# Optimization experiments

Measured on AMD Instinct MI355X. Metric: run time of the kernel, lower is better.

Reference implementation:

```python
import jax, jax.numpy as jnp
import numpy as np

B, C, CI, HM, HC = 4, 64, 32, 128, 64  # batch, in_channels, inter_channels, main HW, cross HW
BN_EPS = 1e-5


def conv1x1(x, w, b):
    # x: [B,Cin,H,W], w: [Cout,Cin], b: [Cout]
    return jnp.einsum('bchw,oc->bohw', x, w) + b[None, :, None, None]


def _lin_coords(n_in, n_out):
    # PyTorch bilinear, align_corners=False: src = (i+0.5)*scale - 0.5, clamped
    scale = n_in / n_out
    src = (jnp.arange(n_out, dtype=jnp.float32) + 0.5) * scale - 0.5
    src = jnp.clip(src, 0.0, n_in - 1)
    i0 = jnp.floor(src).astype(jnp.int32)
    i1 = jnp.minimum(i0 + 1, n_in - 1)
    w = src - i0.astype(jnp.float32)
    return i0, i1, w


def resize_bilinear(x, h_out, w_out):
    # x: [B,C,H,W] -> [B,C,h_out,w_out], matches torch F.interpolate(mode='bilinear', align_corners=False)
    _, _, h_in, w_in = x.shape
    i0, i1, wh = _lin_coords(h_in, h_out)
    x = x[:, :, i0, :] * (1.0 - wh)[None, None, :, None] + x[:, :, i1, :] * wh[None, None, :, None]
    j0, j1, ww = _lin_coords(w_in, w_out)
    x = x[:, :, :, j0] * (1.0 - ww)[None, None, None, :] + x[:, :, :, j1] * ww[None, None, None, :]
    return x


def setup_inputs() -> dict:
    key = jax.random.key(0)
    ks = jax.random.split(key, 12)
    p = lambda k, shape, s=0.05: jax.random.normal(k, shape, dtype=jnp.float32) * s
    return {
        'main_feature': jax.random.normal(ks[0], (B, C, HM, HM), dtype=jnp.float32),
        'cross_feature': jax.random.normal(ks[1], (B, C, HC, HC), dtype=jnp.float32),
        'g_w': p(ks[2], (CI, C)), 'g_b': p(ks[3], (CI,)),
        'theta_w': p(ks[4], (CI, C)), 'theta_b': p(ks[5], (CI,)),
        'phi_w': p(ks[6], (CI, C)), 'phi_b': p(ks[7], (CI,)),
        'w_w': p(ks[8], (C, CI)), 'w_b': p(ks[9], (C,)),
        'bn_gamma': 1.0 + p(ks[10], (C,)), 'bn_beta': p(ks[11], (C,)),
    }


def reference(main_feature, cross_feature, g_w, g_b, theta_w, theta_b,
              phi_w, phi_b, w_w, w_b, bn_gamma, bn_beta):
    b, _, hc, wc = cross_feature.shape
    hm = main_feature.shape[2]
    # g(cross) -> [B, Nc, Ci]
    x = conv1x1(cross_feature, g_w, g_b).reshape(b, CI, -1).transpose(0, 2, 1)
    # theta(cross) -> [B, Ci, Nc]
    y = conv1x1(cross_feature, theta_w, theta_b).reshape(b, CI, -1)
    # phi(resize(main -> cross size)) -> [B, Nc, Ci]
    z = resize_bilinear(main_feature, hc, hc)
    z = conv1x1(z, phi_w, phi_b).reshape(b, CI, -1).transpose(0, 2, 1)
    # unscaled attention: [B, Nc, Nc]
    f = jnp.einsum('bnc,bcm->bnm', x, y)
    attn = jax.nn.softmax(f, axis=-1)
    out = jnp.einsum('bnm,bmc->bnc', attn, z)           # [B, Nc, Ci]
    out = out.transpose(0, 2, 1).reshape(b, CI, hc, wc)  # [B, Ci, Hc, Wc]
    # W: 1x1 conv + BatchNorm2d (training mode: batch statistics, biased var)
    out = conv1x1(out, w_w, w_b)
    mean = out.mean(axis=(0, 2, 3), keepdims=True)
    var = out.var(axis=(0, 2, 3), keepdims=True)
    out = (out - mean) * jax.lax.rsqrt(var + BN_EPS)
    out = out * bn_gamma[None, :, None, None] + bn_beta[None, :, None, None]
    out = resize_bilinear(out, hm, hm)
    return out + main_feature
```

## Files before the change

### kernel.cpp

```cpp
#include <hip/hip_runtime.h>
#include <hip/hip_bf16.h>


typedef __attribute__((ext_vector_type(8))) short bf16x8;
typedef __attribute__((ext_vector_type(4))) float f32x4;
typedef __attribute__((ext_vector_type(16))) float f32x16;

#define LOG2E 1.4426950408889634f

static __device__ __forceinline__ unsigned short f2bf_bits(float x) {
    __hip_bfloat16 h = __float2bfloat16(x);
    return *(unsigned short*)&h;
}
static __device__ __forceinline__ unsigned int pk2bf(float a, float b) {
    __hip_bfloat162 h = __float22bfloat162_rn(make_float2(a, b));
    return *(unsigned int*)&h;
}

__global__ __launch_bounds__(256) void qkv_kernel(
    const float* __restrict__ cross, const float* __restrict__ mainf,
    const float* __restrict__ g_w,  const float* __restrict__ g_b,
    const float* __restrict__ th_w, const float* __restrict__ th_b,
    const float* __restrict__ ph_w, const float* __restrict__ ph_b,
    __hip_bfloat16* __restrict__ Qb, __hip_bfloat16* __restrict__ Kb,
    __hip_bfloat16* __restrict__ Vt)
{
    __shared__ float xs[64][128];
    const int kind = blockIdx.x >> 7;
    const int sub  = blockIdx.x & 127;
    const int b    = sub >> 5;
    const int n0   = (sub & 31) << 7;
    const int tid  = threadIdx.x;
    const float* w  = (kind == 0) ? g_w : (kind == 1) ? th_w : ph_w;
    const float* bs = (kind == 0) ? g_b : (kind == 1) ? th_b : ph_b;

    if (kind < 2) {
        const float* src = cross + (((size_t)(b * 64)) << 12) + n0;
        const int jr = (tid & 31) << 2, c0 = tid >> 5;
#pragma unroll
        for (int it = 0; it < 8; ++it) {
            int c = (it << 3) | c0;
            *(float4*)&xs[c][jr] = *(const float4*)(src + ((size_t)c << 12) + jr);
        }
    } else {
        const int px = tid & 127, chh = tid >> 7;
        const int n = n0 + px;
        const int i2 = (n >> 6) << 1, j2 = (n & 63) << 1;
        const float* src = mainf + (((size_t)(b * 64)) << 14) + i2 * 128 + j2;
#pragma unroll 4
        for (int cc = 0; cc < 32; ++cc) {
            int c = (chh << 5) | cc;
            const float2 a = *(const float2*)(src + ((size_t)c << 14));
            const float2 d = *(const float2*)(src + ((size_t)c << 14) + 128);
            xs[c][px] = 0.25f * ((a.x + a.y) + (d.x + d.y));
        }
    }
    __syncthreads();

    const int px = tid & 127, cih = tid >> 7, ci0 = cih << 4;
    float acc[16];
#pragma unroll
    for (int j = 0; j < 16; ++j) acc[j] = bs[ci0 + j];
#pragma unroll 4
    for (int c = 0; c < 64; ++c) {
        float x = xs[c][px];
#pragma unroll
        for (int j = 0; j < 16; ++j)
            acc[j] = fmaf(w[((ci0 + j) << 6) + c], x, acc[j]);
    }
    const int n = n0 + px;
    const int pix = (b << 12) + n;
    if (kind < 2) {
        if (kind == 0) {
#pragma unroll
            for (int j = 0; j < 16; ++j) acc[j] *= LOG2E;
        }
        unsigned int u[8];
#pragma unroll
        for (int i = 0; i < 8; ++i)
            u[i] = (unsigned int)f2bf_bits(acc[2 * i]) |
                   ((unsigned int)f2bf_bits(acc[2 * i + 1]) << 16);
        uint4* d4 = (uint4*)(((kind == 0) ? Qb : Kb) + (size_t)pix * 32 + ci0);
        d4[0] = make_uint4(u[0], u[1], u[2], u[3]);
        d4[1] = make_uint4(u[4], u[5], u[6], u[7]);
    } else {
#pragma unroll
        for (int j = 0; j < 16; ++j)
            Vt[((size_t)((b << 5) | (ci0 + j)) << 12) + n] = __float2bfloat16(acc[j]);
    }
}

__global__ __launch_bounds__(256) void attn_part(
    const __hip_bfloat16* __restrict__ Qb, const __hip_bfloat16* __restrict__ Kb,
    const __hip_bfloat16* __restrict__ Vt,
    float* __restrict__ pnum, float* __restrict__ pden)
{
    __shared__ __align__(16) float redbuf[3][64][20];
    const int tid = threadIdx.x, lane = tid & 63, w = tid >> 6;
    const int q = lane & 31, h = lane >> 5;
    const int b = blockIdx.y, qbase = blockIdx.x << 5, half = blockIdx.z;
    const int sig = (q & ~12) | ((q & 4) << 1) | ((q & 8) >> 1);

    const __hip_bfloat16* Qrow = Qb + (((size_t)(b << 12) + qbase + q) << 5);
    const bf16x8 bq1 = *(const bf16x8*)(Qrow + 8 * h);
    const bf16x8 bq2 = *(const bf16x8*)(Qrow + 16 + 8 * h);

    const __hip_bfloat16* Kbb = Kb + ((size_t)(b << 12) << 5);
    const __hip_bfloat16* Vbb = Vt + ((size_t)(b << 5) << 12) + ((size_t)q << 12);
    const int kq = (half << 11) + (w << 9);
#define LDK1(k) (*(const bf16x8*)(Kbb + ((size_t)((k) + sig) << 5) + 8 * h))
#define LDK2(k) (*(const bf16x8*)(Kbb + ((size_t)((k) + sig) << 5) + 16 + 8 * h))
#define LDV1(k) (*(const bf16x8*)(Vbb + (k) + 8 * h))
#define LDV2(k) (*(const bf16x8*)(Vbb + (k) + 16 + 8 * h))

    f32x16 acc;
#pragma unroll
    for (int r = 0; r < 16; ++r) acc[r] = 0.f;
    const f32x16 z16 = acc;
    float den = 0.f;

    bf16x8 a1c = LDK1(kq),      a2c = LDK2(kq);
    bf16x8 v1B = LDV1(kq),      v2B = LDV2(kq);
    bf16x8 a1n = LDK1(kq + 32), a2n = LDK2(kq + 32);
    bf16x8 v1N = LDV1(kq + 32), v2N = LDV2(kq + 32);
    bf16x8 ap1, ap2, v1A, v2A;

    {
        f32x16 s = __builtin_amdgcn_mfma_f32_32x32x16_bf16(a1c, bq1, z16, 0, 0, 0);
        s = __builtin_amdgcn_mfma_f32_32x32x16_bf16(a2c, bq2, s, 0, 0, 0);
        float e[16];
#pragma unroll
        for (int r = 0; r < 16; ++r) e[r] = __builtin_amdgcn_exp2f(s[r]);
        den += (((e[0]+e[1])+(e[2]+e[3])) + ((e[4]+e[5])+(e[6]+e[7])))
             + (((e[8]+e[9])+(e[10]+e[11])) + ((e[12]+e[13])+(e[14]+e[15])));
        uint4 t1 = make_uint4(pk2bf(e[0],e[1]), pk2bf(e[2],e[3]),
                              pk2bf(e[4],e[5]), pk2bf(e[6],e[7]));
        uint4 t2 = make_uint4(pk2bf(e[8],e[9]), pk2bf(e[10],e[11]),
                              pk2bf(e[12],e[13]), pk2bf(e[14],e[15]));
        ap1 = *(bf16x8*)&t1; ap2 = *(bf16x8*)&t2;
    }

#pragma unroll 2
    for (int ch = 1; ch < 16; ++ch) {
        const int kn = kq + ((ch + 1) & 15) * 32;
        v1A = v1B; v2A = v2B;
        v1B = v1N; v2B = v2N;
        a1c = a1n; a2c = a2n;
        a1n = LDK1(kn); a2n = LDK2(kn);
        v1N = LDV1(kn); v2N = LDV2(kn);

        f32x16 s = __builtin_amdgcn_mfma_f32_32x32x16_bf16(a1c, bq1, z16, 0, 0, 0);
        s = __builtin_amdgcn_mfma_f32_32x32x16_bf16(a2c, bq2, s, 0, 0, 0);

        acc = __builtin_amdgcn_mfma_f32_32x32x16_bf16(ap1, v1A, acc, 0, 0, 0);
        acc = __builtin_amdgcn_mfma_f32_32x32x16_bf16(ap2, v2A, acc, 0, 0, 0);

        float e[16];
#pragma unroll
        for (int r = 0; r < 16; ++r) e[r] = __builtin_amdgcn_exp2f(s[r]);
        den += (((e[0]+e[1])+(e[2]+e[3])) + ((e[4]+e[5])+(e[6]+e[7])))
             + (((e[8]+e[9])+(e[10]+e[11])) + ((e[12]+e[13])+(e[14]+e[15])));
        uint4 t1 = make_uint4(pk2bf(e[0],e[1]), pk2bf(e[2],e[3]),
                              pk2bf(e[4],e[5]), pk2bf(e[6],e[7]));
        uint4 t2 = make_uint4(pk2bf(e[8],e[9]), pk2bf(e[10],e[11]),
                              pk2bf(e[12],e[13]), pk2bf(e[14],e[15]));
        ap1 = *(bf16x8*)&t1; ap2 = *(bf16x8*)&t2;
    }
    acc = __builtin_amdgcn_mfma_f32_32x32x16_bf16(ap1, v1B, acc, 0, 0, 0);
    acc = __builtin_amdgcn_mfma_f32_32x32x16_bf16(ap2, v2B, acc, 0, 0, 0);
#undef LDK1
#undef LDK2
#undef LDV1
#undef LDV2

    den += __shfl_xor(den, 32);

    if (w) {
        float* rb = &redbuf[w - 1][lane][0];
        f32x4* rb4 = (f32x4*)rb;
#pragma unroll
        for (int p = 0; p < 4; ++p) {
            f32x4 t = {acc[4*p], acc[4*p+1], acc[4*p+2], acc[4*p+3]};
            rb4[p] = t;
        }
        rb[16] = den;
    }
    __syncthreads();
    if (w == 0) {
#pragma unroll
        for (int ww = 0; ww < 3; ++ww) {
            const float* rb = &redbuf[ww][lane][0];
            const f32x4* rb4 = (const f32x4*)rb;
#pragma unroll
            for (int p = 0; p < 4; ++p) {
                f32x4 t = rb4[p];
                acc[4*p] += t[0]; acc[4*p+1] += t[1];
                acc[4*p+2] += t[2]; acc[4*p+3] += t[3];
            }
            den += rb[16];
        }
        const int tile = (((half << 2) | b) << 7) | blockIdx.x;
        float* pn = pnum + ((size_t)tile << 10);
#pragma unroll
        for (int r = 0; r < 16; ++r) {
            int qr = (r & 3) + 8 * (r >> 2) + 4 * h;
            pn[(qr << 5) + q] = acc[r];
        }
        if (h == 0) pden[(tile << 5) + q] = den;
    }
}

__global__ __launch_bounds__(256) void attn_combine(
    const float* __restrict__ pnum, const float* __restrict__ pden,
    const float* __restrict__ w_w, const float* __restrict__ w_b,
    float* __restrict__ out2)
{
    __shared__ __align__(16) float obuf[32][36];
    const int tid = threadIdx.x;
    const int b = blockIdx.y, qbase = blockIdx.x << 5;
    const int tile0 = ((b) << 7) | blockIdx.x;
    const int tile1 = ((4 + b) << 7) | blockIdx.x;

    const float* pn0 = pnum + ((size_t)tile0 << 10);
    const float* pn1 = pnum + ((size_t)tile1 << 10);
#pragma unroll
    for (int k = 0; k < 4; ++k) {
        int e = tid + (k << 8);
        int qr = e >> 5, ci = e & 31;
        float num = pn0[e] + pn1[e];
        float den = pden[(tile0 << 5) + qr] + pden[(tile1 << 5) + qr];
        obuf[qr][ci] = num * (1.0f / den);
    }
    __syncthreads();

    const int qq = tid & 31, cog = tid >> 5;
    float ov[32];
    const float4* orow = (const float4*)&obuf[qq][0];
#pragma unroll
    for (int k4 = 0; k4 < 8; ++k4) {
        float4 t = orow[k4];
        ov[4*k4] = t.x; ov[4*k4+1] = t.y; ov[4*k4+2] = t.z; ov[4*k4+3] = t.w;
    }
    float* dstbase = out2 + (((size_t)(b << 6)) << 12) + qbase + qq;
#pragma unroll
    for (int kk = 0; kk < 8; ++kk) {
        int co = (kk << 3) | cog;
        const float4* wr = (const float4*)&w_w[co << 5];
        float acc2 = w_b[co];
#pragma unroll
        for (int k4 = 0; k4 < 8; ++k4) {
            float4 t = wr[k4];
            acc2 = fmaf(t.x, ov[4*k4],   acc2);
            acc2 = fmaf(t.y, ov[4*k4+1], acc2);
            acc2 = fmaf(t.z, ov[4*k4+2], acc2);
            acc2 = fmaf(t.w, ov[4*k4+3], acc2);
        }
        dstbase[(size_t)co << 12] = acc2;
    }
}

__global__ __launch_bounds__(256) void stats_kernel(
    const float* __restrict__ out2, float* __restrict__ stats1)
{
    int co = blockIdx.x >> 2, b = blockIdx.x & 3, t = threadIdx.x;
    const float* p = out2 + ((size_t)((b << 6) | co) << 12);
    float s = 0.f, s2 = 0.f;
#pragma unroll
    for (int ii = 0; ii < 16; ++ii) {
        float v = p[(ii << 8) | t];
        s += v; s2 = fmaf(v, v, s2);
    }
    __shared__ float rs[256], rs2[256];
    rs[t] = s; rs2[t] = s2;
    __syncthreads();
    for (int off = 128; off > 0; off >>= 1) {
        if (t < off) { rs[t] += rs[t + off]; rs2[t] += rs2[t + off]; }
        __syncthreads();
    }
    if (t == 0) {
        stats1[blockIdx.x * 2]     = rs[0];
        stats1[blockIdx.x * 2 + 1] = rs2[0];
    }
}

__global__ __launch_bounds__(256) void up_kernel(
    const float* __restrict__ out2, const float* __restrict__ stats1,
    const float* __restrict__ gamma, const float* __restrict__ beta,
    const float* __restrict__ mainf, float* __restrict__ out)
{
    int gid = blockIdx.x * 256 + threadIdx.x;
    int j4 = (gid & 31) << 2;
    int i  = (gid >> 5) & 127;
    int co = (gid >> 12) & 63;
    int b  = gid >> 18;

    float sm = 0.f, sq = 0.f;
#pragma unroll
    for (int bb = 0; bb < 4; ++bb) {
        sm += stats1[((co << 2) | bb) * 2];
        sq += stats1[((co << 2) | bb) * 2 + 1];
    }
    float mean = sm * (1.0f / 16384.0f);
    float var  = sq * (1.0f / 16384.0f) - mean * mean;
    float inv  = rsqrtf(var + 1e-5f);
    float scale = gamma[co] * inv;
    float shift = beta[co] - mean * scale;

    int ih = i >> 1;
    int k0, k1; float wi;
    if (i & 1)       { k0 = ih;     k1 = (ih < 63) ? ih + 1 : 63; wi = 0.25f; }
    else if (ih == 0){ k0 = 0;      k1 = 0;                       wi = 0.0f;  }
    else             { k0 = ih - 1; k1 = ih;                      wi = 0.75f; }

    const float* p0r = out2 + ((size_t)((b << 6) | co) << 12) + (k0 << 6);
    const float* p1r = out2 + ((size_t)((b << 6) | co) << 12) + (k1 << 6);

    float res[4];
#pragma unroll
    for (int jj = 0; jj < 4; ++jj) {
        int j = j4 | jj;
        int il = j >> 1;
        int l0, l1; float wj;
        if (j & 1)       { l0 = il;     l1 = (il < 63) ? il + 1 : 63; wj = 0.25f; }
        else if (il == 0){ l0 = 0;      l1 = 0;                       wj = 0.0f;  }
        else             { l0 = il - 1; l1 = il;                      wj = 0.75f; }
        float v00 = p0r[l0], v01 = p0r[l1];
        float v10 = p1r[l0], v11 = p1r[l1];
        float top = v00 + wj * (v01 - v00);
        float bot = v10 + wj * (v11 - v10);
        float v = top + wi * (bot - top);
        res[jj] = fmaf(v, scale, shift);
    }
    size_t idx = (((size_t)((b << 6) | co)) << 14) + (i << 7) + j4;
    float4 m4 = *(const float4*)(mainf + idx);
    *(float4*)(out + idx) = make_float4(res[0] + m4.x, res[1] + m4.y,
                                        res[2] + m4.z, res[3] + m4.w);
}

extern "C" void kernel_launch(void* const* d_in, const int* in_sizes, int n_in,
                              void* d_out, int out_size, void* d_ws, size_t ws_size,
                              hipStream_t stream)
{
    const float* mainf = (const float*)d_in[0];
    const float* cross = (const float*)d_in[1];
    const float* g_w   = (const float*)d_in[2];
    const float* g_b   = (const float*)d_in[3];
    const float* th_w  = (const float*)d_in[4];
    const float* th_b  = (const float*)d_in[5];
    const float* ph_w  = (const float*)d_in[6];
    const float* ph_b  = (const float*)d_in[7];
    const float* w_w   = (const float*)d_in[8];
    const float* w_b   = (const float*)d_in[9];
    const float* gamma = (const float*)d_in[10];
    const float* beta  = (const float*)d_in[11];
    float* out = (float*)d_out;

    __hip_bfloat16* Qb = (__hip_bfloat16*)d_ws;
    __hip_bfloat16* Kb = Qb + 524288;
    __hip_bfloat16* Vt = Kb + 524288;
    float* out2   = (float*)(Vt + 524288);
    float* stats1 = out2 + 1048576;
    float* pnum   = stats1 + 512;
    float* pden   = pnum + 1048576;

    qkv_kernel<<<384, 256, 0, stream>>>(cross, mainf, g_w, g_b, th_w, th_b,
                                        ph_w, ph_b, Qb, Kb, Vt);
    attn_part<<<dim3(128, 4, 2), 256, 0, stream>>>(Qb, Kb, Vt, pnum, pden);
    attn_combine<<<dim3(128, 4), 256, 0, stream>>>(pnum, pden, w_w, w_b, out2);
    stats_kernel<<<256, 256, 0, stream>>>(out2, stats1);
    up_kernel<<<4096, 256, 0, stream>>>(out2, stats1, gamma, beta, mainf, out);
}
```

Baseline: 151.8 us.

## Process two query tiles per attention block and fold BN stats into combine via atomics

The attention partial kernel now handles 64 queries per block in two 32-row tiles that share each K/V load, which halves K/V traffic and the grid size. The separate BN statistics kernel is removed: attn_combine reduces per-channel sum and sum-of-squares with wave shuffles and atomically adds them into a buffer that qkv_kernel zeroes. This saves a kernel launch and a reread of out2, at the cost of higher register pressure in attn_part, fewer blocks in flight, and nondeterministic float atomic ordering.

```diff
diff --git a/kernel.cpp b/kernel.cpp
--- a/kernel.cpp
+++ b/kernel.cpp
@@ -15,6 +15,21 @@
 static __device__ __forceinline__ unsigned int pk2bf(float a, float b) {
     __hip_bfloat162 h = __float22bfloat162_rn(make_float2(a, b));
     return *(unsigned int*)&h;
+}
+
+static __device__ __forceinline__ void softmax_pack(
+    const f32x16& s, float& den, bf16x8& ap1, bf16x8& ap2)
+{
+    float e[16];
+#pragma unroll
+    for (int r = 0; r < 16; ++r) e[r] = __builtin_amdgcn_exp2f(s[r]);
+    den += (((e[0]+e[1])+(e[2]+e[3])) + ((e[4]+e[5])+(e[6]+e[7])))
+         + (((e[8]+e[9])+(e[10]+e[11])) + ((e[12]+e[13])+(e[14]+e[15])));
+    uint4 t1 = make_uint4(pk2bf(e[0],e[1]), pk2bf(e[2],e[3]),
+                          pk2bf(e[4],e[5]), pk2bf(e[6],e[7]));
+    uint4 t2 = make_uint4(pk2bf(e[8],e[9]), pk2bf(e[10],e[11]),
+                          pk2bf(e[12],e[13]), pk2bf(e[14],e[15]));
+    ap1 = *(bf16x8*)&t1; ap2 = *(bf16x8*)&t2;
 }
 
 __global__ __launch_bounds__(256) void qkv_kernel(
@@ -23,7 +38,7 @@
     const float* __restrict__ th_w, const float* __restrict__ th_b,
     const float* __restrict__ ph_w, const float* __restrict__ ph_b,
     __hip_bfloat16* __restrict__ Qb, __hip_bfloat16* __restrict__ Kb,
-    __hip_bfloat16* __restrict__ Vt)
+    __hip_bfloat16* __restrict__ Vt, float* __restrict__ stats1)
 {
     __shared__ float xs[64][128];
     const int kind = blockIdx.x >> 7;
@@ -33,6 +48,8 @@
     const int tid  = threadIdx.x;
     const float* w  = (kind == 0) ? g_w : (kind == 1) ? th_w : ph_w;
     const float* bs = (kind == 0) ? g_b : (kind == 1) ? th_b : ph_b;
+
+    if (blockIdx.x == 0 && tid < 128) stats1[tid] = 0.f;
 
     if (kind < 2) {
         const float* src = cross + (((size_t)(b * 64)) << 12) + n0;
@@ -98,12 +115,15 @@
     __shared__ __align__(16) float redbuf[3][64][20];
     const int tid = threadIdx.x, lane = tid & 63, w = tid >> 6;
     const int q = lane & 31, h = lane >> 5;
-    const int b = blockIdx.y, qbase = blockIdx.x << 5, half = blockIdx.z;
+    const int b = blockIdx.y, qbase = blockIdx.x << 6, half = blockIdx.z;
     const int sig = (q & ~12) | ((q & 4) << 1) | ((q & 8) >> 1);
 
-    const __hip_bfloat16* Qrow = Qb + (((size_t)(b << 12) + qbase + q) << 5);
-    const bf16x8 bq1 = *(const bf16x8*)(Qrow + 8 * h);
-    const bf16x8 bq2 = *(const bf16x8*)(Qrow + 16 + 8 * h);
+    const __hip_bfloat16* QrowA = Qb + (((size_t)(b << 12) + qbase + q) << 5);
+    const bf16x8 bq1A = *(const bf16x8*)(QrowA + 8 * h);
+    const bf16x8 bq2A = *(const bf16x8*)(QrowA + 16 + 8 * h);
+    const __hip_bfloat16* QrowB = QrowA + (32 << 5);
+    const bf16x8 bq1B = *(const bf16x8*)(QrowB + 8 * h);
+    const bf16x8 bq2B = *(const bf16x8*)(QrowB + 16 + 8 * h);
 
     const __hip_bfloat16* Kbb = Kb + ((size_t)(b << 12) << 5);
     const __hip_bfloat16* Vbb = Vt + ((size_t)(b << 5) << 12) + ((size_t)q << 12);
@@ -113,77 +133,72 @@
 #define LDV1(k) (*(const bf16x8*)(Vbb + (k) + 8 * h))
 #define LDV2(k) (*(const bf16x8*)(Vbb + (k) + 16 + 8 * h))
 
-    f32x16 acc;
-#pragma unroll
-    for (int r = 0; r < 16; ++r) acc[r] = 0.f;
-    const f32x16 z16 = acc;
-    float den = 0.f;
+    f32x16 accA, accB;
+#pragma unroll
+    for (int r = 0; r < 16; ++r) { accA[r] = 0.f; accB[r] = 0.f; }
+    const f32x16 z16 = accA;
+    float denA = 0.f, denB = 0.f;
 
     bf16x8 a1c = LDK1(kq),      a2c = LDK2(kq);
-    bf16x8 v1B = LDV1(kq),      v2B = LDV2(kq);
+    bf16x8 vb1 = LDV1(kq),      vb2 = LDV2(kq);
     bf16x8 a1n = LDK1(kq + 32), a2n = LDK2(kq + 32);
-    bf16x8 v1N = LDV1(kq + 32), v2N = LDV2(kq + 32);
-    bf16x8 ap1, ap2, v1A, v2A;
+    bf16x8 vn1 = LDV1(kq + 32), vn2 = LDV2(kq + 32);
+    bf16x8 apA1, apA2, apB1, apB2, vp1, vp2;
 
     {
-        f32x16 s = __builtin_amdgcn_mfma_f32_32x32x16_bf16(a1c, bq1, z16, 0, 0, 0);
-        s = __builtin_amdgcn_mfma_f32_32x32x16_bf16(a2c, bq2, s, 0, 0, 0);
-        float e[16];
-#pragma unroll
-        for (int r = 0; r < 16; ++r) e[r] = __builtin_amdgcn_exp2f(s[r]);
-        den += (((e[0]+e[1])+(e[2]+e[3])) + ((e[4]+e[5])+(e[6]+e[7])))
-             + (((e[8]+e[9])+(e[10]+e[11])) + ((e[12]+e[13])+(e[14]+e[15])));
-        uint4 t1 = make_uint4(pk2bf(e[0],e[1]), pk2bf(e[2],e[3]),
-                              pk2bf(e[4],e[5]), pk2bf(e[6],e[7]));
-        uint4 t2 = make_uint4(pk2bf(e[8],e[9]), pk2bf(e[10],e[11]),
-                              pk2bf(e[12],e[13]), pk2bf(e[14],e[15]));
-        ap1 = *(bf16x8*)&t1; ap2 = *(bf16x8*)&t2;
+        f32x16 sA = __builtin_amdgcn_mfma_f32_32x32x16_bf16(a1c, bq1A, z16, 0, 0, 0);
+        sA = __builtin_amdgcn_mfma_f32_32x32x16_bf16(a2c, bq2A, sA, 0, 0, 0);
+        f32x16 sB = __builtin_amdgcn_mfma_f32_32x32x16_bf16(a1c, bq1B, z16, 0, 0, 0);
+        sB = __builtin_amdgcn_mfma_f32_32x32x16_bf16(a2c, bq2B, sB, 0, 0, 0);
+        softmax_pack(sA, denA, apA1, apA2);
+        softmax_pack(sB, denB, apB1, apB2);
     }
 
 #pragma unroll 2
     for (int ch = 1; ch < 16; ++ch) {
         const int kn = kq + ((ch + 1) & 15) * 32;
-        v1A = v1B; v2A = v2B;
-        v1B = v1N; v2B = v2N;
+        vp1 = vb1; vp2 = vb2;
+        vb1 = vn1; vb2 = vn2;
         a1c = a1n; a2c = a2n;
         a1n = LDK1(kn); a2n = LDK2(kn);
-        v1N = LDV1(kn); v2N = LDV2(kn);
-
-        f32x16 s = __builtin_amdgcn_mfma_f32_32x32x16_bf16(a1c, bq1, z16, 0, 0, 0);
-        s = __builtin_amdgcn_mfma_f32_32x32x16_bf16(a2c, bq2, s, 0, 0, 0);
-
-        acc = __builtin_amdgcn_mfma_f32_32x32x16_bf16(ap1, v1A, acc, 0, 0, 0);
-        acc = __builtin_amdgcn_mfma_f32_32x32x16_bf16(ap2, v2A, acc, 0, 0, 0);
-
-        float e[16];
-#pragma unroll
-        for (int r = 0; r < 16; ++r) e[r] = __builtin_amdgcn_exp2f(s[r]);
-        den += (((e[0]+e[1])+(e[2]+e[3])) + ((e[4]+e[5])+(e[6]+e[7])))
-             + (((e[8]+e[9])+(e[10]+e[11])) + ((e[12]+e[13])+(e[14]+e[15])));
-        uint4 t1 = make_uint4(pk2bf(e[0],e[1]), pk2bf(e[2],e[3]),
-                              pk2bf(e[4],e[5]), pk2bf(e[6],e[7]));
-        uint4 t2 = make_uint4(pk2bf(e[8],e[9]), pk2bf(e[10],e[11]),
-                              pk2bf(e[12],e[13]), pk2bf(e[14],e[15]));
-        ap1 = *(bf16x8*)&t1; ap2 = *(bf16x8*)&t2;
-    }
-    acc = __builtin_amdgcn_mfma_f32_32x32x16_bf16(ap1, v1B, acc, 0, 0, 0);
-    acc = __builtin_amdgcn_mfma_f32_32x32x16_bf16(ap2, v2B, acc, 0, 0, 0);
+        vn1 = LDV1(kn); vn2 = LDV2(kn);
+
+        f32x16 sA = __builtin_amdgcn_mfma_f32_32x32x16_bf16(a1c, bq1A, z16, 0, 0, 0);
+        sA = __builtin_amdgcn_mfma_f32_32x32x16_bf16(a2c, bq2A, sA, 0, 0, 0);
+        f32x16 sB = __builtin_amdgcn_mfma_f32_32x32x16_bf16(a1c, bq1B, z16, 0, 0, 0);
+        sB = __builtin_amdgcn_mfma_f32_32x32x16_bf16(a2c, bq2B, sB, 0, 0, 0);
+
+        accA = __builtin_amdgcn_mfma_f32_32x32x16_bf16(apA1, vp1, accA, 0, 0, 0);
+        accA = __builtin_amdgcn_mfma_f32_32x32x16_bf16(apA2, vp2, accA, 0, 0, 0);
+        accB = __builtin_amdgcn_mfma_f32_32x32x16_bf16(apB1, vp1, accB, 0, 0, 0);
+        accB = __builtin_amdgcn_mfma_f32_32x32x16_bf16(apB2, vp2, accB, 0, 0, 0);
+
+        softmax_pack(sA, denA, apA1, apA2);
+        softmax_pack(sB, denB, apB1, apB2);
+    }
+    accA = __builtin_amdgcn_mfma_f32_32x32x16_bf16(apA1, vb1, accA, 0, 0, 0);
+    accA = __builtin_amdgcn_mfma_f32_32x32x16_bf16(apA2, vb2, accA, 0, 0, 0);
+    accB = __builtin_amdgcn_mfma_f32_32x32x16_bf16(apB1, vb1, accB, 0, 0, 0);
+    accB = __builtin_amdgcn_mfma_f32_32x32x16_bf16(apB2, vb2, accB, 0, 0, 0);
 #undef LDK1
 #undef LDK2
 #undef LDV1
 #undef LDV2
 
-    den += __shfl_xor(den, 32);
+    denA += __shfl_xor(denA, 32);
+    denB += __shfl_xor(denB, 32);
+
+    const int tileA = (((half << 2) | b) << 7) | (blockIdx.x << 1);
 
     if (w) {
         float* rb = &redbuf[w - 1][lane][0];
         f32x4* rb4 = (f32x4*)rb;
 #pragma unroll
         for (int p = 0; p < 4; ++p) {
-            f32x4 t = {acc[4*p], acc[4*p+1], acc[4*p+2], acc[4*p+3]};
+            f32x4 t = {accA[4*p], accA[4*p+1], accA[4*p+2], accA[4*p+3]};
             rb4[p] = t;
         }
-        rb[16] = den;
+        rb[16] = denA;
     }
     __syncthreads();
     if (w == 0) {
@@ -194,26 +209,59 @@
 #pragma unroll
             for (int p = 0; p < 4; ++p) {
                 f32x4 t = rb4[p];
-                acc[4*p] += t[0]; acc[4*p+1] += t[1];
-                acc[4*p+2] += t[2]; acc[4*p+3] += t[3];
+                accA[4*p] += t[0]; accA[4*p+1] += t[1];
+                accA[4*p+2] += t[2]; accA[4*p+3] += t[3];
             }
-            den += rb[16];
-        }
-        const int tile = (((half << 2) | b) << 7) | blockIdx.x;
-        float* pn = pnum + ((size_t)tile << 10);
+            denA += rb[16];
+        }
+        float* pn = pnum + ((size_t)tileA << 10);
 #pragma unroll
         for (int r = 0; r < 16; ++r) {
             int qr = (r & 3) + 8 * (r >> 2) + 4 * h;
-            pn[(qr << 5) + q] = acc[r];
-        }
-        if (h == 0) pden[(tile << 5) + q] = den;
+            pn[(qr << 5) + q] = accA[r];
+        }
+        if (h == 0) pden[(tileA << 5) + q] = denA;
+    }
+    __syncthreads();
+
+    if (w) {
+        float* rb = &redbuf[w - 1][lane][0];
+        f32x4* rb4 = (f32x4*)rb;
+#pragma unroll
+        for (int p = 0; p < 4; ++p) {
+            f32x4 t = {accB[4*p], accB[4*p+1], accB[4*p+2], accB[4*p+3]};
+            rb4[p] = t;
+        }
+        rb[16] = denB;
+    }
+    __syncthreads();
+    if (w == 0) {
+#pragma unroll
+        for (int ww = 0; ww < 3; ++ww) {
+            const float* rb = &redbuf[ww][lane][0];
+            const f32x4* rb4 = (const f32x4*)rb;
+#pragma unroll
+            for (int p = 0; p < 4; ++p) {
+                f32x4 t = rb4[p];
+                accB[4*p] += t[0]; accB[4*p+1] += t[1];
+                accB[4*p+2] += t[2]; accB[4*p+3] += t[3];
+            }
+            denB += rb[16];
+        }
+        float* pn = pnum + ((size_t)(tileA | 1) << 10);
+#pragma unroll
+        for (int r = 0; r < 16; ++r) {
+            int qr = (r & 3) + 8 * (r >> 2) + 4 * h;
+            pn[(qr << 5) + q] = accB[r];
+        }
+        if (h == 0) pden[((tileA | 1) << 5) + q] = denB;
     }
 }
 
 __global__ __launch_bounds__(256) void attn_combine(
     const float* __restrict__ pnum, const float* __restrict__ pden,
     const float* __restrict__ w_w, const float* __restrict__ w_b,
-    float* __restrict__ out2)
+    float* __restrict__ out2, float* __restrict__ stats1)
 {
     __shared__ __align__(16) float obuf[32][36];
     const int tid = threadIdx.x;
@@ -256,30 +304,16 @@
             acc2 = fmaf(t.w, ov[4*k4+3], acc2);
         }
         dstbase[(size_t)co << 12] = acc2;
-    }
-}
-
-__global__ __launch_bounds__(256) void stats_kernel(
-    const float* __restrict__ out2, float* __restrict__ stats1)
-{
-    int co = blockIdx.x >> 2, b = blockIdx.x & 3, t = threadIdx.x;
-    const float* p = out2 + ((size_t)((b << 6) | co) << 12);
-    float s = 0.f, s2 = 0.f;
-#pragma unroll
-    for (int ii = 0; ii < 16; ++ii) {
-        float v = p[(ii << 8) | t];
-        s += v; s2 = fmaf(v, v, s2);
-    }
-    __shared__ float rs[256], rs2[256];
-    rs[t] = s; rs2[t] = s2;
-    __syncthreads();
-    for (int off = 128; off > 0; off >>= 1) {
-        if (t < off) { rs[t] += rs[t + off]; rs2[t] += rs2[t + off]; }
-        __syncthreads();
-    }
-    if (t == 0) {
-        stats1[blockIdx.x * 2]     = rs[0];
-        stats1[blockIdx.x * 2 + 1] = rs2[0];
+        float s1 = acc2, s2 = acc2 * acc2;
+#pragma unroll
+        for (int m = 1; m < 32; m <<= 1) {
+            s1 += __shfl_xor(s1, m);
+            s2 += __shfl_xor(s2, m);
+        }
+        if (qq == 0) {
+            atomicAdd(&stats1[co << 1], s1);
+            atomicAdd(&stats1[(co << 1) | 1], s2);
+        }
     }
 }
 
@@ -294,12 +328,8 @@
     int co = (gid >> 12) & 63;
     int b  = gid >> 18;
 
-    float sm = 0.f, sq = 0.f;
-#pragma unroll
-    for (int bb = 0; bb < 4; ++bb) {
-        sm += stats1[((co << 2) | bb) * 2];
-        sq += stats1[((co << 2) | bb) * 2 + 1];
-    }
+    float sm = stats1[co << 1];
+    float sq = stats1[(co << 1) | 1];
     float mean = sm * (1.0f / 16384.0f);
     float var  = sq * (1.0f / 16384.0f) - mean * mean;
     float inv  = rsqrtf(var + 1e-5f);
@@ -364,9 +394,8 @@
     float* pden   = pnum + 1048576;
 
     qkv_kernel<<<384, 256, 0, stream>>>(cross, mainf, g_w, g_b, th_w, th_b,
-                                        ph_w, ph_b, Qb, Kb, Vt);
-    attn_part<<<dim3(128, 4, 2), 256, 0, stream>>>(Qb, Kb, Vt, pnum, pden);
-    attn_combine<<<dim3(128, 4), 256, 0, stream>>>(pnum, pden, w_w, w_b, out2);
-    stats_kernel<<<256, 256, 0, stream>>>(out2, stats1);
+                                        ph_w, ph_b, Qb, Kb, Vt, stats1);
+    attn_part<<<dim3(64, 4, 2), 256, 0, stream>>>(Qb, Kb, Vt, pnum, pden);
+    attn_combine<<<dim3(128, 4), 256, 0, stream>>>(pnum, pden, w_w, w_b, out2, stats1);
     up_kernel<<<4096, 256, 0, stream>>>(out2, stats1, gamma, beta, mainf, out);
 }
```

Result: slower. 306.9 us (+102.1%).
